# Optimization experiments

Measured on AMD Instinct MI355X. Metric: run time of the kernel, lower is better.

## Reference

```python
import jax, jax.numpy as jnp
import numpy as np

N, D, IN, HID, OUT, E = 20000, 8, 64, 128, 64, 100000
EPS = 1e-5


def _bn(h, g, b):
    # training-mode BatchNorm1d: biased batch variance, eps=1e-5
    m = h.mean(axis=0)
    v = jnp.mean((h - m) ** 2, axis=0)
    return (h - m) * jax.lax.rsqrt(v + EPS) * g + b


def setup_inputs() -> dict:
    key = jax.random.key(0)
    ks = jax.random.split(key, 12)
    x = jax.random.normal(ks[0], (N, IN), dtype=jnp.float32)
    node_ts = jax.random.uniform(ks[1], (N,), dtype=jnp.float32)
    neighbor_idx = jax.random.randint(ks[2], (N, D), 0, N, dtype=jnp.int32)
    neighbor_ts = jax.random.uniform(ks[3], (N, D), dtype=jnp.float32)
    target = jax.random.randint(ks[4], (2, E), 0, N, dtype=jnp.int32)
    neg_pairs = jax.random.randint(ks[5], (2, E), 0, N, dtype=jnp.int32)
    W1 = jax.random.normal(ks[6], (IN, HID), dtype=jnp.float32) * (1.0 / np.sqrt(IN))
    b1 = jnp.zeros((HID,), jnp.float32)
    g1 = jnp.ones((HID,), jnp.float32)
    be1 = jnp.zeros((HID,), jnp.float32)
    W2 = jax.random.normal(ks[7], (HID, OUT), dtype=jnp.float32) * (1.0 / np.sqrt(HID))
    b2 = jnp.zeros((OUT,), jnp.float32)
    g2 = jnp.ones((OUT,), jnp.float32)
    be2 = jnp.zeros((OUT,), jnp.float32)
    Wd = jax.random.normal(ks[8], (OUT, 1), dtype=jnp.float32) * (1.0 / np.sqrt(OUT))
    bd = jnp.zeros((1,), jnp.float32)
    return {"x": x, "node_ts": node_ts, "neighbor_idx": neighbor_idx,
            "neighbor_ts": neighbor_ts, "target": target, "neg_pairs": neg_pairs,
            "W1": W1, "b1": b1, "g1": g1, "be1": be1,
            "W2": W2, "b2": b2, "g2": g2, "be2": be2, "Wd": Wd, "bd": bd}


def reference(x, node_ts, neighbor_idx, neighbor_ts, target, neg_pairs,
              W1, b1, g1, be1, W2, b2, g2, be2, Wd, bd):
    n = jnp.arange(N, dtype=neighbor_idx.dtype)
    # ---- level-2 queries: every node at its own timestamp ----
    # children = D temporal-neighbor slots + self (self always valid, ts=node_ts)
    c_idx = jnp.concatenate([neighbor_idx, n[:, None]], axis=1)          # [N, D+1]
    c_ts = jnp.concatenate([neighbor_ts, node_ts[:, None]], axis=1)      # [N, D+1]
    mask2 = jnp.concatenate([neighbor_ts <= node_ts[:, None],
                             jnp.ones((N, 1), bool)], axis=1)            # [N, D+1]
    # ---- level-1 queries: each (child node, child ts) pair ----
    ci = c_idx.reshape(-1)                                               # [M]
    cts = c_ts.reshape(-1)
    gc_idx = jnp.concatenate([neighbor_idx[ci], ci[:, None]], axis=1)    # [M, D+1]
    mask1 = jnp.concatenate([neighbor_ts[ci] <= cts[:, None],
                             jnp.ones((ci.shape[0], 1), bool)], axis=1)
    # ---- layer 0: raw features of grandchildren ----
    h0 = x[gc_idx]                                                       # [M, D+1, IN]
    m1 = mask1.astype(x.dtype)
    agg1 = jnp.einsum('mk,mkf->mf', m1, h0) / m1.sum(1, keepdims=True)   # masked mean
    h1 = jax.nn.relu(_bn(agg1 @ W1 + b1, g1, be1))                       # [M, HID]
    h1 = h1.reshape(N, D + 1, HID)
    # ---- layer 2 aggregation over temporal children ----
    m2 = mask2.astype(x.dtype)
    agg2 = jnp.einsum('nk,nkf->nf', m2, h1) / m2.sum(1, keepdims=True)
    embs = jax.nn.relu(_bn(agg2 @ W2 + b2, g2, be2))                     # [N, OUT]
    # ---- HadNet link decoder + BCEWithLogits ----
    pos = (embs[target[0]] * embs[target[1]]) @ Wd + bd                  # [E, 1]
    neg = (embs[neg_pairs[0]] * embs[neg_pairs[1]]) @ Wd + bd            # [E, 1]
    preds = jnp.concatenate([pos, neg], axis=0)[:, 0]                    # [2E]
    labels = jnp.concatenate([jnp.ones((E,), x.dtype), jnp.zeros((E,), x.dtype)])
    loss = jnp.mean(jnp.maximum(preds, 0.0) - preds * labels
                    + jnp.log1p(jnp.exp(-jnp.abs(preds))))
    return loss
```

## Files before the change

### kernel.cpp

```cpp
#include <hip/hip_runtime.h>
#include <math.h>

constexpr int kN = 20000;
constexpr int kD = 8;
constexpr int kE = 100000;
constexpr int kM = kN * 9;
constexpr int kTiles1 = kM / 16;
constexpr int kTilesN = kN / 16;
constexpr float kEps = 1e-5f;

constexpr int S_SUM1 = 0, S_SQ1 = 128, S_SUM2 = 256, S_SQ2 = 320;

constexpr size_t OFF_M     = 0;
constexpr size_t OFF_PRE2  = 23040000;
constexpr size_t OFF_STATS = 25600000;
constexpr size_t OFF_CNT   = 25601536;
constexpr size_t OFF_RI    = 26321536;

typedef short short8 __attribute__((ext_vector_type(8)));
typedef float floatx4 __attribute__((ext_vector_type(4)));

__device__ __forceinline__ unsigned f2bf(float f) {
  unsigned u = __float_as_uint(f);
  u += 0x7fffu + ((u >> 16) & 1u);
  return u >> 16;
}

__device__ __forceinline__ void lds_barrier() {
  asm volatile("s_waitcnt lgkmcnt(0)" ::: "memory");
  __builtin_amdgcn_s_barrier();
}

__global__ __launch_bounds__(256) void k0_prefix(
    const float* __restrict__ x, const float* __restrict__ node_ts,
    const int* __restrict__ nidx, const float* __restrict__ nts,
    unsigned short* __restrict__ M, int* __restrict__ rowinfo,
    float* __restrict__ cntf, float* __restrict__ out)
{
  if (blockIdx.x == 0 && threadIdx.x == 0) *out = 0.f;

  int c = blockIdx.x * 4 + (threadIdx.x >> 6);
  const int lane = threadIdx.x & 63;
  c = __builtin_amdgcn_readfirstlane(c);

  float4 t0 = *(const float4*)&nts[c * kD];
  float4 t1 = *(const float4*)&nts[c * kD + 4];
  int4   i0 = *(const int4*)&nidx[c * kD];
  int4   i1 = *(const int4*)&nidx[c * kD + 4];
  float ts[8] = {t0.x, t0.y, t0.z, t0.w, t1.x, t1.y, t1.z, t1.w};
  int   id[8] = {i0.x, i0.y, i0.z, i0.w, i1.x, i1.y, i1.z, i1.w};

#define CSWAP(A, B)                                                   \
  { float ta = ts[A], tb = ts[B]; int ia = id[A], ib = id[B];         \
    bool sw = tb < ta;                                                \
    ts[A] = sw ? tb : ta; ts[B] = sw ? ta : tb;                       \
    id[A] = sw ? ib : ia; id[B] = sw ? ia : ib; }
  CSWAP(0, 1) CSWAP(2, 3) CSWAP(0, 2) CSWAP(1, 3) CSWAP(1, 2)
  CSWAP(4, 5) CSWAP(6, 7) CSWAP(4, 6) CSWAP(5, 7) CSWAP(5, 6)
  CSWAP(0, 4) CSWAP(1, 5) CSWAP(2, 6) CSWAP(3, 7)
  CSWAP(2, 4) CSWAP(3, 5)
  CSWAP(1, 2) CSWAP(3, 4) CSWAP(5, 6)
#undef CSWAP

  float s = x[c * 64 + lane];
  unsigned short* mp = M + (size_t)c * 9 * 64 + lane;
  mp[0] = (unsigned short)f2bf(s);
#pragma unroll
  for (int r = 1; r <= kD; ++r) {
    s += x[id[r - 1] * 64 + lane];
    mp[r * 64] = (unsigned short)f2bf(s / (float)(r + 1));
  }

  const int m = blockIdx.x * 256 + threadIdx.x;
  if (m < kM) {
    const int n = (int)((unsigned)m / 9u);
    const int slot = m - n * 9;
    int cc; float t;
    if (slot < kD) { cc = nidx[n * kD + slot]; t = nts[n * kD + slot]; }
    else           { cc = n;                   t = node_ts[n]; }
    float4 a = *(const float4*)&nts[cc * kD];
    float4 b = *(const float4*)&nts[cc * kD + 4];
    int rank = (a.x <= t) + (a.y <= t) + (a.z <= t) + (a.w <= t)
             + (b.x <= t) + (b.y <= t) + (b.z <= t) + (b.w <= t);
    rowinfo[m] = cc * 9 + rank;
    atomicAdd(&cntf[cc * 9 + rank], 1.0f);
  }
}

__global__ __launch_bounds__(256, 3) void k1_stats(
    const unsigned short* __restrict__ M, const float* __restrict__ cntf,
    const float* __restrict__ W1, const float* __restrict__ b1,
    float* __restrict__ stats)
{
  __shared__ unsigned short W1T[128 * 72];
  __shared__ float redS[256][8];
  __shared__ float redQ[256][8];

  const int tid = threadIdx.x;
  const int lane = tid & 63;
  const int wave = tid >> 6;
  const int l15 = lane & 15;
  const int q = lane >> 4;

  for (int i = tid; i < 8192; i += 256) {
    int n = i >> 6, k = i & 63;
    W1T[n * 72 + k] = (unsigned short)f2bf(W1[k * 128 + n]);
  }
  __syncthreads();

  short8 bf[8][2];
#pragma unroll
  for (int cc = 0; cc < 8; ++cc)
#pragma unroll
    for (int s = 0; s < 2; ++s)
      bf[cc][s] = *(const short8*)&W1T[(cc * 16 + l15) * 72 + q * 8 + s * 32];

  float b1c[8];
#pragma unroll
  for (int cc = 0; cc < 8; ++cc) b1c[cc] = b1[cc * 16 + l15];

  float sum8[8], sq8[8];
#pragma unroll
  for (int cc = 0; cc < 8; ++cc) { sum8[cc] = 0.f; sq8[cc] = 0.f; }

  const int gw = blockIdx.x * 4 + wave;
  const int nw = gridDim.x * 4;

  for (int t = gw; t < kTiles1; t += nw) {
    const unsigned short* mp = M + (size_t)(t * 16 + l15) * 64;
    short8 af0 = *(const short8*)(mp + q * 8);
    short8 af1 = *(const short8*)(mp + 32 + q * 8);
    float c4[4];
#pragma unroll
    for (int i = 0; i < 4; ++i) c4[i] = cntf[t * 16 + q * 4 + i];

    floatx4 acc[8];
#pragma unroll
    for (int cc = 0; cc < 8; ++cc) {
      acc[cc] = (floatx4){0.f, 0.f, 0.f, 0.f};
      acc[cc] = __builtin_amdgcn_mfma_f32_16x16x32_bf16(af0, bf[cc][0], acc[cc], 0, 0, 0);
      acc[cc] = __builtin_amdgcn_mfma_f32_16x16x32_bf16(af1, bf[cc][1], acc[cc], 0, 0, 0);
    }
#pragma unroll
    for (int cc = 0; cc < 8; ++cc) {
#pragma unroll
      for (int i = 0; i < 4; ++i) {
        float v = acc[cc][i] + b1c[cc];
        sum8[cc] += c4[i] * v;
        sq8[cc]  += c4[i] * v * v;
      }
    }
  }

  __syncthreads();
#pragma unroll
  for (int cc = 0; cc < 8; ++cc) { redS[tid][cc] = sum8[cc]; redQ[tid][cc] = sq8[cc]; }
  __syncthreads();
  if (tid < 128) {
    int cc = tid >> 4, r15 = tid & 15;
    float s = 0.f, qq = 0.f;
#pragma unroll
    for (int w = 0; w < 4; ++w)
#pragma unroll
      for (int p = 0; p < 4; ++p) {
        int T = w * 64 + p * 16 + r15;
        s += redS[T][cc]; qq += redQ[T][cc];
      }
    atomicAdd(&stats[S_SUM1 + tid], s);
    atomicAdd(&stats[S_SQ1 + tid], qq);
  }
}

__global__ __launch_bounds__(256, 2) void k3_fused(
    const unsigned short* __restrict__ M, const int* __restrict__ rowinfo,
    const float* __restrict__ node_ts, const float* __restrict__ nts,
    const float* __restrict__ stats_in, const float* __restrict__ g1,
    const float* __restrict__ be1, const float* __restrict__ W1,
    const float* __restrict__ b1, const float* __restrict__ W2,
    const float* __restrict__ b2, float* __restrict__ stats_out,
    unsigned short* __restrict__ pre2)
{
  __shared__ __attribute__((aligned(16))) unsigned short W1T[128 * 72];
  __shared__ __attribute__((aligned(16))) unsigned short W2T[64 * 136];
  __shared__ __attribute__((aligned(16))) unsigned short sm[144 * 132];
  __shared__ __attribute__((aligned(16))) unsigned short aggT[16 * 136];
  __shared__ float wlds[144];
  __shared__ float winv[16];

  const int tid = threadIdx.x;
  const int lane = tid & 63;
  const int wave = tid >> 6;
  const int l15 = lane & 15;
  const int q = lane >> 4;

  int tb = blockIdx.x;
  int ri0 = rowinfo[tb * 144 + wave * 16 + l15];
  int ri1 = rowinfo[tb * 144 + 64 + wave * 16 + l15];
  int ri2 = 0;
  if (wave == 0) ri2 = rowinfo[tb * 144 + 128 + l15];

  for (int i = tid; i < 8192; i += 256) {
    int nn = i >> 6, k = i & 63;
    W1T[nn * 72 + k] = (unsigned short)f2bf(W1[k * 128 + nn]);
  }
  for (int i = tid; i < 8192; i += 256) {
    int nn = i >> 7, k = i & 127;
    W2T[nn * 136 + k] = (unsigned short)f2bf(W2[k * 64 + nn]);
  }
  __syncthreads();

  short8 bf[8][2];
  float scc[8], shc[8];
#pragma unroll
  for (int cc = 0; cc < 8; ++cc) {
    int col = cc * 16 + l15;
#pragma unroll
    for (int s = 0; s < 2; ++s)
      bf[cc][s] = *(const short8*)&W1T[col * 72 + q * 8 + s * 32];
    float mean = stats_in[S_SUM1 + col] * (1.f / kM);
    float var  = stats_in[S_SQ1 + col] * (1.f / kM) - mean * mean;
    float sg   = g1[col] * rsqrtf(var + kEps);
    scc[cc] = sg;
    shc[cc] = (b1[col] - mean) * sg + be1[col];
  }
  short8 bfr2[4];
#pragma unroll
  for (int s = 0; s < 4; ++s)
    bfr2[s] = *(const short8*)&W2T[(wave * 16 + l15) * 136 + q * 8 + s * 32];
  const float b2w = b2[wave * 16 + l15];

  short8 a00, a01, a10, a11;
  short8 a20 = short8{}, a21 = short8{};
  {
    const unsigned short* mp0 = M + (size_t)ri0 * 64;
    const unsigned short* mp1 = M + (size_t)ri1 * 64;
    a00 = *(const short8*)(mp0 + q * 8);
    a01 = *(const short8*)(mp0 + 32 + q * 8);
    a10 = *(const short8*)(mp1 + q * 8);
    a11 = *(const short8*)(mp1 + 32 + q * 8);
    if (wave == 0) {
      const unsigned short* mp2 = M + (size_t)ri2 * 64;
      a20 = *(const short8*)(mp2 + q * 8);
      a21 = *(const short8*)(mp2 + 32 + q * 8);
    }
  }
  if (tb + (int)gridDim.x < kTilesN) {
    int ntb = tb + gridDim.x;
    ri0 = rowinfo[ntb * 144 + wave * 16 + l15];
    ri1 = rowinfo[ntb * 144 + 64 + wave * 16 + l15];
    if (wave == 0) ri2 = rowinfo[ntb * 144 + 128 + l15];
  }

  float sumS = 0.f, sumQ = 0.f;

  for (; tb < kTilesN; tb += gridDim.x) {
    const int node0 = tb * 16;

    if (tid < 144) {
      int ln = tid / 9;
      int slot = tid - ln * 9;
      int nn = node0 + ln;
      float w = 1.f;
      if (slot < kD) w = (nts[nn * kD + slot] <= node_ts[nn]) ? 1.f : 0.f;
      wlds[tid] = w;
    }
    lds_barrier();
    if (tid < 16) {
      float swv = 0.f;
#pragma unroll
      for (int r = 0; r < 9; ++r) swv += wlds[tid * 9 + r];
      winv[tid] = 1.f / swv;
    }

#define ROWTILE(TL, A0, A1)                                                  \
    {                                                                        \
      floatx4 acc[8];                                                        \
      _Pragma("unroll")                                                      \
      for (int cc = 0; cc < 8; ++cc) {                                       \
        acc[cc] = (floatx4){0.f, 0.f, 0.f, 0.f};                             \
        acc[cc] = __builtin_amdgcn_mfma_f32_16x16x32_bf16(A0, bf[cc][0], acc[cc], 0, 0, 0); \
        acc[cc] = __builtin_amdgcn_mfma_f32_16x16x32_bf16(A1, bf[cc][1], acc[cc], 0, 0, 0); \
      }                                                                      \
      float w4[4];                                                           \
      _Pragma("unroll")                                                      \
      for (int i = 0; i < 4; ++i) w4[i] = wlds[(TL) * 16 + q * 4 + i];       \
      _Pragma("unroll")                                                      \
      for (int cc = 0; cc < 8; ++cc) {                                       \
        int col = cc * 16 + l15;                                             \
        _Pragma("unroll")                                                    \
        for (int i = 0; i < 4; ++i) {                                        \
          float val = fmaxf(fmaf(acc[cc][i], scc[cc], shc[cc]), 0.f) * w4[i];\
          sm[((TL) * 16 + q * 4 + i) * 132 + col] = (unsigned short)f2bf(val);\
        }                                                                    \
      }                                                                      \
    }
    ROWTILE(wave, a00, a01)
    ROWTILE(wave + 4, a10, a11)
    if (wave == 0) ROWTILE(8, a20, a21)
#undef ROWTILE

    if (tb + (int)gridDim.x < kTilesN) {
      const unsigned short* mp0 = M + (size_t)ri0 * 64;
      const unsigned short* mp1 = M + (size_t)ri1 * 64;
      a00 = *(const short8*)(mp0 + q * 8);
      a01 = *(const short8*)(mp0 + 32 + q * 8);
      a10 = *(const short8*)(mp1 + q * 8);
      a11 = *(const short8*)(mp1 + 32 + q * 8);
      if (wave == 0) {
        const unsigned short* mp2 = M + (size_t)ri2 * 64;
        a20 = *(const short8*)(mp2 + q * 8);
        a21 = *(const short8*)(mp2 + 32 + q * 8);
      }
      int nntb = tb + 2 * gridDim.x;
      if (nntb < kTilesN) {
        ri0 = rowinfo[nntb * 144 + wave * 16 + l15];
        ri1 = rowinfo[nntb * 144 + 64 + wave * 16 + l15];
        if (wave == 0) ri2 = rowinfo[nntb * 144 + 128 + l15];
      }
    }

    lds_barrier();

#pragma unroll
    for (int k = 0; k < 4; ++k) {
      int it = tid + k * 256;
      int nd = it >> 6, cp = it & 63;
      float s0 = 0.f, s1 = 0.f;
#pragma unroll
      for (int r = 0; r < 9; ++r) {
        unsigned u = *(const unsigned*)&sm[(nd * 9 + r) * 132 + cp * 2];
        s0 += __uint_as_float(u << 16);
        s1 += __uint_as_float(u & 0xffff0000u);
      }
      float iv = winv[nd];
      *(unsigned*)&aggT[nd * 136 + cp * 2] = f2bf(s0 * iv) | (f2bf(s1 * iv) << 16);
    }
    lds_barrier();

    short8 af2[4];
#pragma unroll
    for (int s = 0; s < 4; ++s)
      af2[s] = *(const short8*)&aggT[l15 * 136 + q * 8 + s * 32];
    floatx4 acc2 = (floatx4){0.f, 0.f, 0.f, 0.f};
#pragma unroll
    for (int s = 0; s < 4; ++s)
      acc2 = __builtin_amdgcn_mfma_f32_16x16x32_bf16(af2[s], bfr2[s], acc2, 0, 0, 0);
#pragma unroll
    for (int i = 0; i < 4; ++i) {
      float v = acc2[i] + b2w;
      int nrow = node0 + q * 4 + i;
      pre2[(size_t)nrow * 64 + wave * 16 + l15] = (unsigned short)f2bf(v);
      sumS += v; sumQ += v * v;
    }
  }

  sumS += __shfl_xor(sumS, 16); sumS += __shfl_xor(sumS, 32);
  sumQ += __shfl_xor(sumQ, 16); sumQ += __shfl_xor(sumQ, 32);
  if (lane < 16) {
    atomicAdd(&stats_out[S_SUM2 + wave * 16 + lane], sumS);
    atomicAdd(&stats_out[S_SQ2 + wave * 16 + lane], sumQ);
  }
}

__global__ __launch_bounds__(256) void k6_loss(
    const unsigned short* __restrict__ pre2, const float* __restrict__ stats,
    const float* __restrict__ g2, const float* __restrict__ be2,
    const float* __restrict__ Wd, const int* __restrict__ tgt,
    const int* __restrict__ neg, const float* __restrict__ bd,
    float* __restrict__ out)
{
  __shared__ float scl[64], shl[64], wdl[64];
  __shared__ float redl[256];
  const int tid = threadIdx.x;
  if (tid < 64) {
    float mean = stats[S_SUM2 + tid] * (1.f / kN);
    float var  = stats[S_SQ2 + tid] * (1.f / kN) - mean * mean;
    float s    = g2[tid] * rsqrtf(var + kEps);
    scl[tid] = s; shl[tid] = be2[tid] - mean * s; wdl[tid] = Wd[tid];
  }
  __syncthreads();

  const int tq = tid & 15;
  const int qb = tid >> 4;
  const int c0 = tq * 4;
  const float4 sc4 = {scl[c0], scl[c0 + 1], scl[c0 + 2], scl[c0 + 3]};
  const float4 sh4 = {shl[c0], shl[c0 + 1], shl[c0 + 2], shl[c0 + 3]};
  const float4 wd4 = {wdl[c0], wdl[c0 + 1], wdl[c0 + 2], wdl[c0 + 3]};
  const float bd0 = bd[0];

  float lsum = 0.f;
  const int e0 = blockIdx.x * 128 + qb * 8;
#pragma unroll
  for (int it = 0; it < 8; ++it) {
    int e = e0 + it;
    if (e < 2 * kE) {
      int i, j; float lab;
      if (e < kE) { i = tgt[e];      j = tgt[kE + e]; lab = 1.f; }
      else        { i = neg[e - kE]; j = neg[e];      lab = 0.f; }
      uint2 ua = *(const uint2*)&pre2[(size_t)i * 64 + c0];
      uint2 ub = *(const uint2*)&pre2[(size_t)j * 64 + c0];
      float a0 = __uint_as_float(ua.x << 16), a1 = __uint_as_float(ua.x & 0xffff0000u);
      float a2 = __uint_as_float(ua.y << 16), a3 = __uint_as_float(ua.y & 0xffff0000u);
      float b0 = __uint_as_float(ub.x << 16), b1v = __uint_as_float(ub.x & 0xffff0000u);
      float b2v = __uint_as_float(ub.y << 16), b3 = __uint_as_float(ub.y & 0xffff0000u);
      float ei0 = fmaxf(fmaf(a0, sc4.x, sh4.x), 0.f) * wd4.x;
      float ei1 = fmaxf(fmaf(a1, sc4.y, sh4.y), 0.f) * wd4.y;
      float ei2 = fmaxf(fmaf(a2, sc4.z, sh4.z), 0.f) * wd4.z;
      float ei3 = fmaxf(fmaf(a3, sc4.w, sh4.w), 0.f) * wd4.w;
      float ej0 = fmaxf(fmaf(b0, sc4.x, sh4.x), 0.f);
      float ej1 = fmaxf(fmaf(b1v, sc4.y, sh4.y), 0.f);
      float ej2 = fmaxf(fmaf(b2v, sc4.z, sh4.z), 0.f);
      float ej3 = fmaxf(fmaf(b3, sc4.w, sh4.w), 0.f);
      float p = ei0 * ej0 + ei1 * ej1 + ei2 * ej2 + ei3 * ej3;
      p += __shfl_xor(p, 1); p += __shfl_xor(p, 2);
      p += __shfl_xor(p, 4); p += __shfl_xor(p, 8);
      p += bd0;
      float l = fmaxf(p, 0.f) - p * lab + log1pf(expf(-fabsf(p)));
      if (tq == 0) lsum += l;
    }
  }
  redl[tid] = lsum;
  __syncthreads();
  for (int s = 128; s > 0; s >>= 1) {
    if (tid < s) redl[tid] += redl[tid + s];
    __syncthreads();
  }
  if (tid == 0) atomicAdd(out, redl[0] * (1.f / (2 * kE)));
}

extern "C" void kernel_launch(void* const* d_in, const int* in_sizes, int n_in,
                              void* d_out, int out_size, void* d_ws, size_t ws_size,
                              hipStream_t stream) {
  (void)in_sizes; (void)n_in; (void)out_size; (void)ws_size;
  const float* x       = (const float*)d_in[0];
  const float* node_ts = (const float*)d_in[1];
  const int*   nidx    = (const int*)d_in[2];
  const float* nts     = (const float*)d_in[3];
  const int*   tgt     = (const int*)d_in[4];
  const int*   neg     = (const int*)d_in[5];
  const float* W1      = (const float*)d_in[6];
  const float* b1      = (const float*)d_in[7];
  const float* g1      = (const float*)d_in[8];
  const float* be1     = (const float*)d_in[9];
  const float* W2      = (const float*)d_in[10];
  const float* b2      = (const float*)d_in[11];
  const float* g2      = (const float*)d_in[12];
  const float* be2     = (const float*)d_in[13];
  const float* Wd      = (const float*)d_in[14];
  const float* bd      = (const float*)d_in[15];

  char* ws = (char*)d_ws;
  unsigned short* Mbuf = (unsigned short*)(ws + OFF_M);
  unsigned short* pre2 = (unsigned short*)(ws + OFF_PRE2);
  float* stats = (float*)(ws + OFF_STATS);
  float* cntf  = (float*)(ws + OFF_CNT);
  int*   rinfo = (int*)(ws + OFF_RI);
  float* out   = (float*)d_out;

  hipMemsetAsync(ws + OFF_STATS, 0, 1536 + 720000, stream);

  k0_prefix<<<kN / 4, 256, 0, stream>>>(x, node_ts, nidx, nts, Mbuf, rinfo,
                                        cntf, out);
  k1_stats<<<704, 256, 0, stream>>>(Mbuf, cntf, W1, b1, stats);
  k3_fused<<<512, 256, 0, stream>>>(Mbuf, rinfo, node_ts, nts, stats, g1, be1,
                                    W1, b1, W2, b2, stats, pre2);
  k6_loss<<<(2 * kE + 127) / 128, 256, 0, stream>>>(pre2, stats, g2, be2, Wd,
                                                    tgt, neg, bd, out);
}
```

Measured before the change: 199.7 us.

## Fuse stats and main kernels with a software grid barrier

Merges the BN1 statistics kernel and the fused layer kernel into one persistent kernel of 512 blocks, separated by an atomic-counter grid barrier. This removes one launch and lets the W1/W2 bf16 transposition into LDS and the W1 fragment registers be built once and reused across both phases. LDS is shared through one union buffer. It also prefetches the next tile's timestamp-mask inputs so they load while the current tile is being computed. The barrier assumes all 512 blocks are resident at the same time, which depends on occupancy, and the stats phase now runs on fewer blocks (512 instead of 704).

```diff
diff --git a/kernel.cpp b/kernel.cpp
--- a/kernel.cpp
+++ b/kernel.cpp
@@ -8,6 +8,7 @@
 constexpr int kTiles1 = kM / 16;
 constexpr int kTilesN = kN / 16;
 constexpr float kEps = 1e-5f;
+constexpr int kGrid3 = 512;
 
 constexpr int S_SUM1 = 0, S_SQ1 = 128, S_SUM2 = 256, S_SQ2 = 320;
 
@@ -15,7 +16,8 @@
 constexpr size_t OFF_PRE2  = 23040000;
 constexpr size_t OFF_STATS = 25600000;
 constexpr size_t OFF_CNT   = 25601536;
-constexpr size_t OFF_RI    = 26321536;
+constexpr size_t OFF_BAR   = 26321536;
+constexpr size_t OFF_RI    = 26321600;
 
 typedef short short8 __attribute__((ext_vector_type(8)));
 typedef float floatx4 __attribute__((ext_vector_type(4)));
@@ -29,6 +31,18 @@
 __device__ __forceinline__ void lds_barrier() {
   asm volatile("s_waitcnt lgkmcnt(0)" ::: "memory");
   __builtin_amdgcn_s_barrier();
+}
+
+__device__ __forceinline__ void grid_bar(int* bar, int target) {
+  __syncthreads();
+  if (threadIdx.x == 0) {
+    __threadfence();
+    __hip_atomic_fetch_add(bar, 1, __ATOMIC_RELEASE, __HIP_MEMORY_SCOPE_AGENT);
+    while (__hip_atomic_load(bar, __ATOMIC_RELAXED, __HIP_MEMORY_SCOPE_AGENT) < target)
+      __builtin_amdgcn_s_sleep(2);
+    __threadfence();
+  }
+  __syncthreads();
 }
 
 __global__ __launch_bounds__(256) void k0_prefix(
@@ -87,14 +101,24 @@
   }
 }
 
-__global__ __launch_bounds__(256, 3) void k1_stats(
-    const unsigned short* __restrict__ M, const float* __restrict__ cntf,
-    const float* __restrict__ W1, const float* __restrict__ b1,
-    float* __restrict__ stats)
+__global__ __launch_bounds__(256, 2) void k13_fused(
+    const unsigned short* __restrict__ M, const int* __restrict__ rowinfo,
+    const float* __restrict__ cntf, const float* __restrict__ node_ts,
+    const float* __restrict__ nts, const float* __restrict__ g1,
+    const float* __restrict__ be1, const float* __restrict__ W1,
+    const float* __restrict__ b1, const float* __restrict__ W2,
+    const float* __restrict__ b2, float* __restrict__ stats,
+    unsigned short* __restrict__ pre2, int* bar)
 {
-  __shared__ unsigned short W1T[128 * 72];
-  __shared__ float redS[256][8];
-  __shared__ float redQ[256][8];
+  __shared__ __attribute__((aligned(16))) char lds[78848];
+  unsigned short* W1T  = (unsigned short*)lds;
+  unsigned short* W2T  = (unsigned short*)(lds + 18432);
+  unsigned short* sm   = (unsigned short*)(lds + 35840);
+  unsigned short* aggT = (unsigned short*)(lds + 73856);
+  float* wlds = (float*)(lds + 78208);
+  float* winv = (float*)(lds + 78784);
+  float* redS = (float*)(lds + 35840);
+  float* redQ = (float*)(lds + 35840 + 8192);
 
   const int tid = threadIdx.x;
   const int lane = tid & 63;
@@ -103,132 +127,100 @@
   const int q = lane >> 4;
 
   for (int i = tid; i < 8192; i += 256) {
-    int n = i >> 6, k = i & 63;
-    W1T[n * 72 + k] = (unsigned short)f2bf(W1[k * 128 + n]);
+    int nn = i >> 6, k = i & 63;
+    W1T[nn * 72 + k] = (unsigned short)f2bf(W1[k * 128 + nn]);
+  }
+  for (int i = tid; i < 8192; i += 256) {
+    int nn = i >> 7, k = i & 127;
+    W2T[nn * 136 + k] = (unsigned short)f2bf(W2[k * 64 + nn]);
   }
   __syncthreads();
 
   short8 bf[8][2];
-#pragma unroll
-  for (int cc = 0; cc < 8; ++cc)
+  float b1c[8];
+#pragma unroll
+  for (int cc = 0; cc < 8; ++cc) {
+    int col = cc * 16 + l15;
 #pragma unroll
     for (int s = 0; s < 2; ++s)
-      bf[cc][s] = *(const short8*)&W1T[(cc * 16 + l15) * 72 + q * 8 + s * 32];
-
-  float b1c[8];
-#pragma unroll
-  for (int cc = 0; cc < 8; ++cc) b1c[cc] = b1[cc * 16 + l15];
-
-  float sum8[8], sq8[8];
-#pragma unroll
-  for (int cc = 0; cc < 8; ++cc) { sum8[cc] = 0.f; sq8[cc] = 0.f; }
-
-  const int gw = blockIdx.x * 4 + wave;
-  const int nw = gridDim.x * 4;
-
-  for (int t = gw; t < kTiles1; t += nw) {
-    const unsigned short* mp = M + (size_t)(t * 16 + l15) * 64;
-    short8 af0 = *(const short8*)(mp + q * 8);
-    short8 af1 = *(const short8*)(mp + 32 + q * 8);
-    float c4[4];
-#pragma unroll
-    for (int i = 0; i < 4; ++i) c4[i] = cntf[t * 16 + q * 4 + i];
-
-    floatx4 acc[8];
-#pragma unroll
-    for (int cc = 0; cc < 8; ++cc) {
-      acc[cc] = (floatx4){0.f, 0.f, 0.f, 0.f};
-      acc[cc] = __builtin_amdgcn_mfma_f32_16x16x32_bf16(af0, bf[cc][0], acc[cc], 0, 0, 0);
-      acc[cc] = __builtin_amdgcn_mfma_f32_16x16x32_bf16(af1, bf[cc][1], acc[cc], 0, 0, 0);
-    }
-#pragma unroll
-    for (int cc = 0; cc < 8; ++cc) {
-#pragma unroll
-      for (int i = 0; i < 4; ++i) {
-        float v = acc[cc][i] + b1c[cc];
-        sum8[cc] += c4[i] * v;
-        sq8[cc]  += c4[i] * v * v;
+      bf[cc][s] = *(const short8*)&W1T[col * 72 + q * 8 + s * 32];
+    b1c[cc] = b1[col];
+  }
+
+  {
+    float sum8[8], sq8[8];
+#pragma unroll
+    for (int cc = 0; cc < 8; ++cc) { sum8[cc] = 0.f; sq8[cc] = 0.f; }
+
+    const int gw = blockIdx.x * 4 + wave;
+    for (int t = gw; t < kTiles1; t += kGrid3 * 4) {
+      const unsigned short* mp = M + (size_t)(t * 16 + l15) * 64;
+      short8 af0 = *(const short8*)(mp + q * 8);
+      short8 af1 = *(const short8*)(mp + 32 + q * 8);
+      float c4[4];
+#pragma unroll
+      for (int i = 0; i < 4; ++i) c4[i] = cntf[t * 16 + q * 4 + i];
+
+      floatx4 acc[8];
+#pragma unroll
+      for (int cc = 0; cc < 8; ++cc) {
+        acc[cc] = (floatx4){0.f, 0.f, 0.f, 0.f};
+        acc[cc] = __builtin_amdgcn_mfma_f32_16x16x32_bf16(af0, bf[cc][0], acc[cc], 0, 0, 0);
+        acc[cc] = __builtin_amdgcn_mfma_f32_16x16x32_bf16(af1, bf[cc][1], acc[cc], 0, 0, 0);
       }
-    }
-  }
-
-  __syncthreads();
-#pragma unroll
-  for (int cc = 0; cc < 8; ++cc) { redS[tid][cc] = sum8[cc]; redQ[tid][cc] = sq8[cc]; }
-  __syncthreads();
-  if (tid < 128) {
-    int cc = tid >> 4, r15 = tid & 15;
-    float s = 0.f, qq = 0.f;
-#pragma unroll
-    for (int w = 0; w < 4; ++w)
-#pragma unroll
-      for (int p = 0; p < 4; ++p) {
-        int T = w * 64 + p * 16 + r15;
-        s += redS[T][cc]; qq += redQ[T][cc];
+#pragma unroll
+      for (int cc = 0; cc < 8; ++cc) {
+#pragma unroll
+        for (int i = 0; i < 4; ++i) {
+          float v = acc[cc][i] + b1c[cc];
+          sum8[cc] += c4[i] * v;
+          sq8[cc]  += c4[i] * v * v;
+        }
       }
-    atomicAdd(&stats[S_SUM1 + tid], s);
-    atomicAdd(&stats[S_SQ1 + tid], qq);
-  }
-}
-
-__global__ __launch_bounds__(256, 2) void k3_fused(
-    const unsigned short* __restrict__ M, const int* __restrict__ rowinfo,
-    const float* __restrict__ node_ts, const float* __restrict__ nts,
-    const float* __restrict__ stats_in, const float* __restrict__ g1,
-    const float* __restrict__ be1, const float* __restrict__ W1,
-    const float* __restrict__ b1, const float* __restrict__ W2,
-    const float* __restrict__ b2, float* __restrict__ stats_out,
-    unsigned short* __restrict__ pre2)
-{
-  __shared__ __attribute__((aligned(16))) unsigned short W1T[128 * 72];
-  __shared__ __attribute__((aligned(16))) unsigned short W2T[64 * 136];
-  __shared__ __attribute__((aligned(16))) unsigned short sm[144 * 132];
-  __shared__ __attribute__((aligned(16))) unsigned short aggT[16 * 136];
-  __shared__ float wlds[144];
-  __shared__ float winv[16];
-
-  const int tid = threadIdx.x;
-  const int lane = tid & 63;
-  const int wave = tid >> 6;
-  const int l15 = lane & 15;
-  const int q = lane >> 4;
+    }
+
+    __syncthreads();
+#pragma unroll
+    for (int cc = 0; cc < 8; ++cc) { redS[tid * 8 + cc] = sum8[cc]; redQ[tid * 8 + cc] = sq8[cc]; }
+    __syncthreads();
+    if (tid < 128) {
+      int cc = tid >> 4, r15 = tid & 15;
+      float s = 0.f, qq = 0.f;
+#pragma unroll
+      for (int w = 0; w < 4; ++w)
+#pragma unroll
+        for (int p = 0; p < 4; ++p) {
+          int T = w * 64 + p * 16 + r15;
+          s += redS[T * 8 + cc]; qq += redQ[T * 8 + cc];
+        }
+      atomicAdd(&stats[S_SUM1 + tid], s);
+      atomicAdd(&stats[S_SQ1 + tid], qq);
+    }
+  }
+
+  grid_bar(bar, kGrid3);
+
+  float scc[8], shc[8];
+#pragma unroll
+  for (int cc = 0; cc < 8; ++cc) {
+    int col = cc * 16 + l15;
+    float mean = stats[S_SUM1 + col] * (1.f / kM);
+    float var  = stats[S_SQ1 + col] * (1.f / kM) - mean * mean;
+    float sg   = g1[col] * rsqrtf(var + kEps);
+    scc[cc] = sg;
+    shc[cc] = (b1c[cc] - mean) * sg + be1[col];
+  }
+  short8 bfr2[4];
+#pragma unroll
+  for (int s = 0; s < 4; ++s)
+    bfr2[s] = *(const short8*)&W2T[(wave * 16 + l15) * 136 + q * 8 + s * 32];
+  const float b2w = b2[wave * 16 + l15];
 
   int tb = blockIdx.x;
   int ri0 = rowinfo[tb * 144 + wave * 16 + l15];
   int ri1 = rowinfo[tb * 144 + 64 + wave * 16 + l15];
   int ri2 = 0;
   if (wave == 0) ri2 = rowinfo[tb * 144 + 128 + l15];
-
-  for (int i = tid; i < 8192; i += 256) {
-    int nn = i >> 6, k = i & 63;
-    W1T[nn * 72 + k] = (unsigned short)f2bf(W1[k * 128 + nn]);
-  }
-  for (int i = tid; i < 8192; i += 256) {
-    int nn = i >> 7, k = i & 127;
-    W2T[nn * 136 + k] = (unsigned short)f2bf(W2[k * 64 + nn]);
-  }
-  __syncthreads();
-
-  short8 bf[8][2];
-  float scc[8], shc[8];
-#pragma unroll
-  for (int cc = 0; cc < 8; ++cc) {
-    int col = cc * 16 + l15;
-#pragma unroll
-    for (int s = 0; s < 2; ++s)
-      bf[cc][s] = *(const short8*)&W1T[col * 72 + q * 8 + s * 32];
-    float mean = stats_in[S_SUM1 + col] * (1.f / kM);
-    float var  = stats_in[S_SQ1 + col] * (1.f / kM) - mean * mean;
-    float sg   = g1[col] * rsqrtf(var + kEps);
-    scc[cc] = sg;
-    shc[cc] = (b1[col] - mean) * sg + be1[col];
-  }
-  short8 bfr2[4];
-#pragma unroll
-  for (int s = 0; s < 4; ++s)
-    bfr2[s] = *(const short8*)&W2T[(wave * 16 + l15) * 136 + q * 8 + s * 32];
-  const float b2w = b2[wave * 16 + l15];
-
   short8 a00, a01, a10, a11;
   short8 a20 = short8{}, a21 = short8{};
   {
@@ -244,27 +236,36 @@
       a21 = *(const short8*)(mp2 + 32 + q * 8);
     }
   }
-  if (tb + (int)gridDim.x < kTilesN) {
-    int ntb = tb + gridDim.x;
+  if (tb + kGrid3 < kTilesN) {
+    int ntb = tb + kGrid3;
     ri0 = rowinfo[ntb * 144 + wave * 16 + l15];
     ri1 = rowinfo[ntb * 144 + 64 + wave * 16 + l15];
     if (wave == 0) ri2 = rowinfo[ntb * 144 + 128 + l15];
   }
 
+  const int ln9 = (tid < 144) ? (tid / 9) : 0;
+  const int sl9 = (tid < 144) ? (tid - ln9 * 9) : 0;
+  if (tid < 144) {
+    int nn = tb * 16 + ln9;
+    float w = 1.f;
+    if (sl9 < kD) w = (nts[nn * kD + sl9] <= node_ts[nn]) ? 1.f : 0.f;
+    wlds[tid] = w;
+  }
+
   float sumS = 0.f, sumQ = 0.f;
 
-  for (; tb < kTilesN; tb += gridDim.x) {
+  for (; tb < kTilesN; tb += kGrid3) {
     const int node0 = tb * 16;
-
-    if (tid < 144) {
-      int ln = tid / 9;
-      int slot = tid - ln * 9;
-      int nn = node0 + ln;
-      float w = 1.f;
-      if (slot < kD) w = (nts[nn * kD + slot] <= node_ts[nn]) ? 1.f : 0.f;
-      wlds[tid] = w;
-    }
+    const bool have_next = (tb + kGrid3 < kTilesN);
+
     lds_barrier();
+
+    float ntsv = 0.f, tnv = 0.f;
+    if (tid < 144 && have_next) {
+      int nn = (tb + kGrid3) * 16 + ln9;
+      if (sl9 < kD) ntsv = nts[nn * kD + sl9];
+      tnv = node_ts[nn];
+    }
     if (tid < 16) {
       float swv = 0.f;
 #pragma unroll
@@ -299,7 +300,7 @@
     if (wave == 0) ROWTILE(8, a20, a21)
 #undef ROWTILE
 
-    if (tb + (int)gridDim.x < kTilesN) {
+    if (have_next) {
       const unsigned short* mp0 = M + (size_t)ri0 * 64;
       const unsigned short* mp1 = M + (size_t)ri1 * 64;
       a00 = *(const short8*)(mp0 + q * 8);
@@ -311,7 +312,7 @@
         a20 = *(const short8*)(mp2 + q * 8);
         a21 = *(const short8*)(mp2 + 32 + q * 8);
       }
-      int nntb = tb + 2 * gridDim.x;
+      int nntb = tb + 2 * kGrid3;
       if (nntb < kTilesN) {
         ri0 = rowinfo[nntb * 144 + wave * 16 + l15];
         ri1 = rowinfo[nntb * 144 + 64 + wave * 16 + l15];
@@ -320,6 +321,11 @@
     }
 
     lds_barrier();
+
+    if (tid < 144 && have_next) {
+      float w = (sl9 < kD) ? ((ntsv <= tnv) ? 1.f : 0.f) : 1.f;
+      wlds[tid] = w;
+    }
 
 #pragma unroll
     for (int k = 0; k < 4; ++k) {
@@ -357,8 +363,8 @@
   sumS += __shfl_xor(sumS, 16); sumS += __shfl_xor(sumS, 32);
   sumQ += __shfl_xor(sumQ, 16); sumQ += __shfl_xor(sumQ, 32);
   if (lane < 16) {
-    atomicAdd(&stats_out[S_SUM2 + wave * 16 + lane], sumS);
-    atomicAdd(&stats_out[S_SQ2 + wave * 16 + lane], sumQ);
+    atomicAdd(&stats[S_SUM2 + wave * 16 + lane], sumS);
+    atomicAdd(&stats[S_SQ2 + wave * 16 + lane], sumQ);
   }
 }
 
@@ -454,16 +460,17 @@
   unsigned short* pre2 = (unsigned short*)(ws + OFF_PRE2);
   float* stats = (float*)(ws + OFF_STATS);
   float* cntf  = (float*)(ws + OFF_CNT);
+  int*   bar   = (int*)(ws + OFF_BAR);
   int*   rinfo = (int*)(ws + OFF_RI);
   float* out   = (float*)d_out;
 
-  hipMemsetAsync(ws + OFF_STATS, 0, 1536 + 720000, stream);
+  hipMemsetAsync(ws + OFF_STATS, 0, 1536 + 720000 + 64, stream);
 
   k0_prefix<<<kN / 4, 256, 0, stream>>>(x, node_ts, nidx, nts, Mbuf, rinfo,
                                         cntf, out);
-  k1_stats<<<704, 256, 0, stream>>>(Mbuf, cntf, W1, b1, stats);
-  k3_fused<<<512, 256, 0, stream>>>(Mbuf, rinfo, node_ts, nts, stats, g1, be1,
-                                    W1, b1, W2, b2, stats, pre2);
+  k13_fused<<<kGrid3, 256, 0, stream>>>(Mbuf, rinfo, cntf, node_ts, nts,
+                                        g1, be1, W1, b1, W2, b2, stats,
+                                        pre2, bar);
   k6_loss<<<(2 * kE + 127) / 128, 256, 0, stream>>>(pre2, stats, g2, be2, Wd,
                                                     tgt, neg, bd, out);
 }
```

New measurement: 228.9 us. 14.6% more time.
